# Kernel tuning notes

Measured on AMD Instinct MI355X. Metric: run time of the kernel, lower is better.

The kernel has to match this reference:

```python
import jax, jax.numpy as jnp
import numpy as np

B, S, D_IN, D_OUT = 4, 2048, 4096, 4096
ACT_CLIP = 6.0

def setup_inputs() -> dict:
    key = jax.random.key(0)
    k1, k2, k3, k4 = jax.random.split(key, 4)
    x = jax.random.normal(k1, (B, S, D_IN), dtype=jnp.float32)
    # symmetric int8 weights in [-127, 127] (stored as int8)
    weight_i8 = jax.random.randint(k2, (D_OUT, D_IN), -127, 128, dtype=jnp.int32).astype(jnp.int8)
    # per-output-channel positive scales, ~ max|w|/127 magnitude
    weight_scale = (jax.random.uniform(k3, (D_OUT,), dtype=jnp.float32) * 0.02 + 1e-4)
    bias = jax.random.normal(k4, (D_OUT,), dtype=jnp.float32)
    return {"x": x, "weight_i8": weight_i8, "weight_scale": weight_scale, "bias": bias}

def reference(x, weight_i8, weight_scale, bias):
    # activation clip
    x = jnp.clip(x, -ACT_CLIP, ACT_CLIP)
    # per-channel dequant: weight[o, i] = i8[o, i] * scale[o]
    weight = weight_i8.astype(jnp.float32) * weight_scale[:, None]
    weight = weight.astype(x.dtype)
    # F.linear: x @ weight.T + bias
    out = jnp.einsum('bsi,oi->bso', x, weight) + bias.astype(x.dtype)
    return out
```

## Files before the change

### kernel.cpp

```cpp
#include <hip/hip_runtime.h>
#include <stdint.h>
#include <stddef.h>


#define M_DIM 8192
#define N_DIM 4096
#define K_DIM 4096
#define ACT_CLIP 6.0f

#define BM 256
#define BN 128
#define BKI 64
#define NKT (K_DIM / BKI)
#define A_BYTES (BM * BKI)
#define B_BYTES (BN * BKI)
#define TILE_LDS (A_BYTES + B_BYTES)
#define RING 3

typedef __attribute__((ext_vector_type(4))) int i32x4;
typedef __attribute__((ext_vector_type(16))) int i32x16;

__device__ __forceinline__ void async_load16(const void* g, void* l) {
    __builtin_amdgcn_global_load_lds(
        (const __attribute__((address_space(1))) void*)g,
        (__attribute__((address_space(3))) void*)l, 16, 0, 0);
}

__global__ __launch_bounds__(256) void prep_kernel(
    const float* __restrict__ x, int8_t* __restrict__ xq,
    float* __restrict__ rowscale,
    const int* __restrict__ w, int8_t* __restrict__ wq) {
    const int tid = threadIdx.x;
    if (blockIdx.x < M_DIM) {
        const int row = blockIdx.x;
        const float4* xr = (const float4*)(x + (size_t)row * K_DIM);
        float4 v[4];
        float mx = 0.f;
#pragma unroll
        for (int c = 0; c < 4; ++c) {
            float4 a = xr[c * 256 + tid];
            a.x = fminf(ACT_CLIP, fmaxf(-ACT_CLIP, a.x));
            a.y = fminf(ACT_CLIP, fmaxf(-ACT_CLIP, a.y));
            a.z = fminf(ACT_CLIP, fmaxf(-ACT_CLIP, a.z));
            a.w = fminf(ACT_CLIP, fmaxf(-ACT_CLIP, a.w));
            v[c] = a;
            mx = fmaxf(mx, fmaxf(fmaxf(fabsf(a.x), fabsf(a.y)),
                                 fmaxf(fabsf(a.z), fabsf(a.w))));
        }
#pragma unroll
        for (int off = 32; off >= 1; off >>= 1)
            mx = fmaxf(mx, __shfl_xor(mx, off, 64));
        __shared__ float wmax[4];
        if ((tid & 63) == 0) wmax[tid >> 6] = mx;
        __syncthreads();
        mx = fmaxf(fmaxf(wmax[0], wmax[1]), fmaxf(wmax[2], wmax[3]));
        mx = fmaxf(mx, 1e-20f);
        const float inv = 127.f / mx;
        if (tid == 0) rowscale[row] = mx * (1.f / 127.f);
        int* out = (int*)(xq + (size_t)row * K_DIM);
#pragma unroll
        for (int c = 0; c < 4; ++c) {
            int b0 = (int)rintf(v[c].x * inv);
            int b1 = (int)rintf(v[c].y * inv);
            int b2 = (int)rintf(v[c].z * inv);
            int b3 = (int)rintf(v[c].w * inv);
            out[c * 256 + tid] =
                (b0 & 255) | ((b1 & 255) << 8) | ((b2 & 255) << 16) | ((b3 & 255) << 24);
        }
    } else {
        size_t idx = (size_t)(blockIdx.x - M_DIM) * 256 + tid;
        const int4* w4 = (const int4*)w;
        int r[4];
#pragma unroll
        for (int j = 0; j < 4; ++j) {
            int4 a = w4[idx * 4 + j];
            r[j] = (a.x & 255) | ((a.y & 255) << 8) | ((a.z & 255) << 16) |
                   ((a.w & 255) << 24);
        }
        ((int4*)wq)[idx] = make_int4(r[0], r[1], r[2], r[3]);
    }
}

__global__ __launch_bounds__(256, 2) void gemm_i8_kernel(
    const int8_t* __restrict__ A, const int8_t* __restrict__ Bw,
    const float* __restrict__ rowscale, const float* __restrict__ scale,
    const float* __restrict__ bias, float* __restrict__ out) {
    extern __shared__ __align__(16) int8_t smem[];

    const int tid = threadIdx.x;
    const int wave = tid >> 6;
    const int lane = tid & 63;
    const int l31 = lane & 31;
    const int hi = lane >> 5;
    const int m0 = blockIdx.y * BM;
    const int n0 = blockIdx.x * BN;
    const int wm = (wave >> 1) * 128;
    const int wn = (wave & 1) * 64;

    const int8_t* ga[4];
    const int8_t* gb[2];
    int lbA[4], lbB[2];
#pragma unroll
    for (int j = 0; j < 4; ++j) {
        const int s = tid + 256 * j;
        const int row = s >> 2;
        const int c = (s & 3) ^ ((row >> 1) & 3);
        ga[j] = A + (size_t)(m0 + row) * K_DIM + c * 16;
        lbA[j] = (wave * 64 + 256 * j) * 16;
    }
#pragma unroll
    for (int j = 0; j < 2; ++j) {
        const int s = tid + 256 * j;
        const int row = s >> 2;
        const int c = (s & 3) ^ ((row >> 1) & 3);
        gb[j] = Bw + (size_t)(n0 + row) * K_DIM + c * 16;
        lbB[j] = A_BYTES + (wave * 64 + 256 * j) * 16;
    }

    auto STAGE = [&](int b) {
        int8_t* buf = smem + b * TILE_LDS;
#pragma unroll
        for (int j = 0; j < 4; ++j) async_load16(ga[j], buf + lbA[j]);
#pragma unroll
        for (int j = 0; j < 2; ++j) async_load16(gb[j], buf + lbB[j]);
#pragma unroll
        for (int j = 0; j < 4; ++j) ga[j] += BKI;
#pragma unroll
        for (int j = 0; j < 2; ++j) gb[j] += BKI;
    };

    const int swz = (l31 >> 1) & 3;
    const int abase = (wm + l31) * 64;
    const int bbase = A_BYTES + (wn + l31) * 64;
    int koff[2];
#pragma unroll
    for (int ks = 0; ks < 2; ++ks) koff[ks] = ((ks * 2 + hi) ^ swz) * 16;

    i32x16 acc[4][2] = {};

    STAGE(0);
    STAGE(1);
    asm volatile("s_waitcnt vmcnt(6)" ::: "memory");
    asm volatile("s_barrier" ::: "memory");

    int cur = 0, stg = 2;
    for (int t = 0; t < NKT; ++t) {
        if (t + 2 < NKT) STAGE(stg);

        const int8_t* buf = smem + cur * TILE_LDS;
        i32x4 af[4][2], bf[2][2];
#pragma unroll
        for (int ks = 0; ks < 2; ++ks) {
#pragma unroll
            for (int mt = 0; mt < 4; ++mt)
                af[mt][ks] = *(const i32x4*)(buf + abase + mt * 2048 + koff[ks]);
#pragma unroll
            for (int nt = 0; nt < 2; ++nt)
                bf[nt][ks] = *(const i32x4*)(buf + bbase + nt * 2048 + koff[ks]);
        }
#pragma unroll
        for (int ks = 0; ks < 2; ++ks)
#pragma unroll
            for (int mt = 0; mt < 4; ++mt)
#pragma unroll
                for (int nt = 0; nt < 2; ++nt)
                    acc[mt][nt] = __builtin_amdgcn_mfma_i32_32x32x32_i8(
                        af[mt][ks], bf[nt][ks], acc[mt][nt], 0, 0, 0);

        if (t < NKT - 2) {
            asm volatile("s_waitcnt vmcnt(6)" ::: "memory");
            asm volatile("s_barrier" ::: "memory");
        } else if (t == NKT - 2) {
            asm volatile("s_waitcnt vmcnt(0)" ::: "memory");
            asm volatile("s_barrier" ::: "memory");
        }
        cur = (cur == 2) ? 0 : cur + 1;
        stg = (stg == 2) ? 0 : stg + 1;
    }

    const int ccol = l31;
#pragma unroll
    for (int mt = 0; mt < 4; ++mt) {
        const int gmb = m0 + wm + mt * 32;
        float rs[16];
#pragma unroll
        for (int r = 0; r < 16; ++r)
            rs[r] = rowscale[gmb + (r & 3) + 4 * hi + 8 * (r >> 2)];
#pragma unroll
        for (int nt = 0; nt < 2; ++nt) {
            const int gn = n0 + wn + nt * 32 + ccol;
            const float sc = scale[gn];
            const float bi = bias[gn];
            float* op = out + (size_t)gmb * N_DIM + gn;
#pragma unroll
            for (int r = 0; r < 16; ++r) {
                const int grow = (r & 3) + 4 * hi + 8 * (r >> 2);
                op[(size_t)grow * N_DIM] =
                    fmaf((float)acc[mt][nt][r], rs[r] * sc, bi);
            }
        }
    }
}

extern "C" void kernel_launch(void* const* d_in, const int* in_sizes, int n_in,
                              void* d_out, int out_size, void* d_ws, size_t ws_size,
                              hipStream_t stream) {
    const float* x = (const float*)d_in[0];
    const int* w_i8 = (const int*)d_in[1];
    const float* w_scale = (const float*)d_in[2];
    const float* bias = (const float*)d_in[3];
    float* out = (float*)d_out;

    int8_t* xq = (int8_t*)d_ws;
    int8_t* wq = (int8_t*)d_ws + (size_t)M_DIM * K_DIM;
    float* rowscale = (float*)((int8_t*)d_ws + (size_t)M_DIM * K_DIM
                               + (size_t)N_DIM * K_DIM);

    static bool attr_done = false;
    if (!attr_done) {
        hipFuncSetAttribute((const void*)gemm_i8_kernel,
                            hipFuncAttributeMaxDynamicSharedMemorySize,
                            RING * TILE_LDS);
        attr_done = true;
    }

    const int pack_blocks = (int)((size_t)N_DIM * K_DIM / (16 * 256));
    prep_kernel<<<M_DIM + pack_blocks, 256, 0, stream>>>(x, xq, rowscale, w_i8, wq);

    dim3 grid(N_DIM / BN, M_DIM / BM);
    gemm_i8_kernel<<<grid, 256, RING * TILE_LDS, stream>>>(
        xq, wq, rowscale, w_scale, bias, out);
}
```

Before: 413.1 us.

## Pre-tile int8 operands into MFMA fragment layout and load directly to registers

The prep kernel now writes quantized activations and packed weights in a blocked layout: 32-row blocks where each 16-byte lane chunk matches the MFMA operand fragment. The GEMM kernel drops the LDS ring buffer, the async global-to-LDS copies and the barriers. It loads fragments straight from global memory into registers with software double buffering. This removes LDS traffic and synchronisation, but each wave refetches its A/B tiles with no sharing between waves, so L2 and global bandwidth pressure rises.

```diff
diff --git a/kernel.cpp b/kernel.cpp
--- a/kernel.cpp
+++ b/kernel.cpp
@@ -12,19 +12,10 @@
 #define BN 128
 #define BKI 64
 #define NKT (K_DIM / BKI)
-#define A_BYTES (BM * BKI)
-#define B_BYTES (BN * BKI)
-#define TILE_LDS (A_BYTES + B_BYTES)
-#define RING 3
+#define BLK_STRIDE (128 * 1024)
 
 typedef __attribute__((ext_vector_type(4))) int i32x4;
 typedef __attribute__((ext_vector_type(16))) int i32x16;
-
-__device__ __forceinline__ void async_load16(const void* g, void* l) {
-    __builtin_amdgcn_global_load_lds(
-        (const __attribute__((address_space(1))) void*)g,
-        (__attribute__((address_space(3))) void*)l, 16, 0, 0);
-}
 
 __global__ __launch_bounds__(256) void prep_kernel(
     const float* __restrict__ x, int8_t* __restrict__ xq,
@@ -32,13 +23,14 @@
     const int* __restrict__ w, int8_t* __restrict__ wq) {
     const int tid = threadIdx.x;
     if (blockIdx.x < M_DIM) {
-        const int row = blockIdx.x;
+        const int g = blockIdx.x >> 8, i = blockIdx.x & 255;
+        const int row = g * 256 + (i & 7) * 32 + (i >> 3);
         const float4* xr = (const float4*)(x + (size_t)row * K_DIM);
         float4 v[4];
         float mx = 0.f;
 #pragma unroll
         for (int c = 0; c < 4; ++c) {
-            float4 a = xr[c * 256 + tid];
+            float4 a = xr[tid * 4 + c];
             a.x = fminf(ACT_CLIP, fmaxf(-ACT_CLIP, a.x));
             a.y = fminf(ACT_CLIP, fmaxf(-ACT_CLIP, a.y));
             a.z = fminf(ACT_CLIP, fmaxf(-ACT_CLIP, a.z));
@@ -57,36 +49,41 @@
         mx = fmaxf(mx, 1e-20f);
         const float inv = 127.f / mx;
         if (tid == 0) rowscale[row] = mx * (1.f / 127.f);
-        int* out = (int*)(xq + (size_t)row * K_DIM);
+        int bo[4];
 #pragma unroll
         for (int c = 0; c < 4; ++c) {
             int b0 = (int)rintf(v[c].x * inv);
             int b1 = (int)rintf(v[c].y * inv);
             int b2 = (int)rintf(v[c].z * inv);
             int b3 = (int)rintf(v[c].w * inv);
-            out[c * 256 + tid] =
-                (b0 & 255) | ((b1 & 255) << 8) | ((b2 & 255) << 16) | ((b3 & 255) << 24);
+            bo[c] = (b0 & 255) | ((b1 & 255) << 8) | ((b2 & 255) << 16) |
+                    ((b3 & 255) << 24);
         }
+        int8_t* dst = xq + ((size_t)(row >> 5) * 128 + (tid >> 1)) * 1024 +
+                      (row & 31) * 16 + (tid & 1) * 512;
+        *(int4*)dst = make_int4(bo[0], bo[1], bo[2], bo[3]);
     } else {
-        size_t idx = (size_t)(blockIdx.x - M_DIM) * 256 + tid;
-        const int4* w4 = (const int4*)w;
-        int r[4];
+        const int pb = blockIdx.x - M_DIM;
+        const int g = pb >> 8, i = pb & 255;
+        const int n = g * 256 + (i & 7) * 32 + (i >> 3);
+        const int4* w4 = (const int4*)(w + (size_t)n * K_DIM);
+        int bo[4];
 #pragma unroll
         for (int j = 0; j < 4; ++j) {
-            int4 a = w4[idx * 4 + j];
-            r[j] = (a.x & 255) | ((a.y & 255) << 8) | ((a.z & 255) << 16) |
-                   ((a.w & 255) << 24);
+            int4 a = w4[tid * 4 + j];
+            bo[j] = (a.x & 255) | ((a.y & 255) << 8) | ((a.z & 255) << 16) |
+                    ((a.w & 255) << 24);
         }
-        ((int4*)wq)[idx] = make_int4(r[0], r[1], r[2], r[3]);
+        int8_t* dst = wq + ((size_t)(n >> 5) * 128 + (tid >> 1)) * 1024 +
+                      (n & 31) * 16 + (tid & 1) * 512;
+        *(int4*)dst = make_int4(bo[0], bo[1], bo[2], bo[3]);
     }
 }
 
 __global__ __launch_bounds__(256, 2) void gemm_i8_kernel(
-    const int8_t* __restrict__ A, const int8_t* __restrict__ Bw,
+    const int8_t* __restrict__ At, const int8_t* __restrict__ Bt,
     const float* __restrict__ rowscale, const float* __restrict__ scale,
     const float* __restrict__ bias, float* __restrict__ out) {
-    extern __shared__ __align__(16) int8_t smem[];
-
     const int tid = threadIdx.x;
     const int wave = tid >> 6;
     const int lane = tid & 63;
@@ -97,86 +94,55 @@
     const int wm = (wave >> 1) * 128;
     const int wn = (wave & 1) * 64;
 
-    const int8_t* ga[4];
-    const int8_t* gb[2];
-    int lbA[4], lbB[2];
+    const int8_t* pa[4];
+    const int8_t* pb[2];
 #pragma unroll
-    for (int j = 0; j < 4; ++j) {
-        const int s = tid + 256 * j;
-        const int row = s >> 2;
-        const int c = (s & 3) ^ ((row >> 1) & 3);
-        ga[j] = A + (size_t)(m0 + row) * K_DIM + c * 16;
-        lbA[j] = (wave * 64 + 256 * j) * 16;
-    }
+    for (int mt = 0; mt < 4; ++mt)
+        pa[mt] = At + (size_t)(((m0 + wm) >> 5) + mt) * BLK_STRIDE + lane * 16;
 #pragma unroll
-    for (int j = 0; j < 2; ++j) {
-        const int s = tid + 256 * j;
-        const int row = s >> 2;
-        const int c = (s & 3) ^ ((row >> 1) & 3);
-        gb[j] = Bw + (size_t)(n0 + row) * K_DIM + c * 16;
-        lbB[j] = A_BYTES + (wave * 64 + 256 * j) * 16;
-    }
+    for (int nt = 0; nt < 2; ++nt)
+        pb[nt] = Bt + (size_t)(((n0 + wn) >> 5) + nt) * BLK_STRIDE + lane * 16;
 
-    auto STAGE = [&](int b) {
-        int8_t* buf = smem + b * TILE_LDS;
-#pragma unroll
-        for (int j = 0; j < 4; ++j) async_load16(ga[j], buf + lbA[j]);
-#pragma unroll
-        for (int j = 0; j < 2; ++j) async_load16(gb[j], buf + lbB[j]);
-#pragma unroll
-        for (int j = 0; j < 4; ++j) ga[j] += BKI;
-#pragma unroll
-        for (int j = 0; j < 2; ++j) gb[j] += BKI;
-    };
-
-    const int swz = (l31 >> 1) & 3;
-    const int abase = (wm + l31) * 64;
-    const int bbase = A_BYTES + (wn + l31) * 64;
-    int koff[2];
-#pragma unroll
-    for (int ks = 0; ks < 2; ++ks) koff[ks] = ((ks * 2 + hi) ^ swz) * 16;
-
+    i32x4 aX[8], bX[4], aY[8], bY[4];
     i32x16 acc[4][2] = {};
 
-    STAGE(0);
-    STAGE(1);
-    asm volatile("s_waitcnt vmcnt(6)" ::: "memory");
-    asm volatile("s_barrier" ::: "memory");
+#define LOADT(af, bf)                                                  \
+    do {                                                               \
+        _Pragma("unroll") for (int mt = 0; mt < 4; ++mt) {             \
+            af[mt * 2 + 0] = *(const i32x4*)(pa[mt]);                  \
+            af[mt * 2 + 1] = *(const i32x4*)(pa[mt] + 1024);           \
+        }                                                              \
+        _Pragma("unroll") for (int nt = 0; nt < 2; ++nt) {             \
+            bf[nt * 2 + 0] = *(const i32x4*)(pb[nt]);                  \
+            bf[nt * 2 + 1] = *(const i32x4*)(pb[nt] + 1024);           \
+        }                                                              \
+        _Pragma("unroll") for (int mt = 0; mt < 4; ++mt) pa[mt] += 2048; \
+        _Pragma("unroll") for (int nt = 0; nt < 2; ++nt) pb[nt] += 2048; \
+    } while (0)
 
-    int cur = 0, stg = 2;
-    for (int t = 0; t < NKT; ++t) {
-        if (t + 2 < NKT) STAGE(stg);
+#define MFMAT(af, bf)                                                  \
+    do {                                                               \
+        _Pragma("unroll") for (int ks = 0; ks < 2; ++ks)               \
+            _Pragma("unroll") for (int mt = 0; mt < 4; ++mt)           \
+                _Pragma("unroll") for (int nt = 0; nt < 2; ++nt)       \
+                    acc[mt][nt] = __builtin_amdgcn_mfma_i32_32x32x32_i8( \
+                        af[mt * 2 + ks], bf[nt * 2 + ks], acc[mt][nt], \
+                        0, 0, 0);                                      \
+    } while (0)
 
-        const int8_t* buf = smem + cur * TILE_LDS;
-        i32x4 af[4][2], bf[2][2];
-#pragma unroll
-        for (int ks = 0; ks < 2; ++ks) {
-#pragma unroll
-            for (int mt = 0; mt < 4; ++mt)
-                af[mt][ks] = *(const i32x4*)(buf + abase + mt * 2048 + koff[ks]);
-#pragma unroll
-            for (int nt = 0; nt < 2; ++nt)
-                bf[nt][ks] = *(const i32x4*)(buf + bbase + nt * 2048 + koff[ks]);
-        }
-#pragma unroll
-        for (int ks = 0; ks < 2; ++ks)
-#pragma unroll
-            for (int mt = 0; mt < 4; ++mt)
-#pragma unroll
-                for (int nt = 0; nt < 2; ++nt)
-                    acc[mt][nt] = __builtin_amdgcn_mfma_i32_32x32x32_i8(
-                        af[mt][ks], bf[nt][ks], acc[mt][nt], 0, 0, 0);
+    LOADT(aX, bX);
+    for (int t = 0; t < NKT - 2; t += 2) {
+        LOADT(aY, bY);
+        MFMAT(aX, bX);
+        LOADT(aX, bX);
+        MFMAT(aY, bY);
+    }
+    LOADT(aY, bY);
+    MFMAT(aX, bX);
+    MFMAT(aY, bY);
 
-        if (t < NKT - 2) {
-            asm volatile("s_waitcnt vmcnt(6)" ::: "memory");
-            asm volatile("s_barrier" ::: "memory");
-        } else if (t == NKT - 2) {
-            asm volatile("s_waitcnt vmcnt(0)" ::: "memory");
-            asm volatile("s_barrier" ::: "memory");
-        }
-        cur = (cur == 2) ? 0 : cur + 1;
-        stg = (stg == 2) ? 0 : stg + 1;
-    }
+#undef LOADT
+#undef MFMAT
 
     const int ccol = l31;
 #pragma unroll
@@ -216,18 +182,9 @@
     float* rowscale = (float*)((int8_t*)d_ws + (size_t)M_DIM * K_DIM
                                + (size_t)N_DIM * K_DIM);
 
-    static bool attr_done = false;
-    if (!attr_done) {
-        hipFuncSetAttribute((const void*)gemm_i8_kernel,
-                            hipFuncAttributeMaxDynamicSharedMemorySize,
-                            RING * TILE_LDS);
-        attr_done = true;
-    }
-
-    const int pack_blocks = (int)((size_t)N_DIM * K_DIM / (16 * 256));
-    prep_kernel<<<M_DIM + pack_blocks, 256, 0, stream>>>(x, xq, rowscale, w_i8, wq);
+    prep_kernel<<<M_DIM + N_DIM, 256, 0, stream>>>(x, xq, rowscale, w_i8, wq);
 
     dim3 grid(N_DIM / BN, M_DIM / BM);
-    gemm_i8_kernel<<<grid, 256, RING * TILE_LDS, stream>>>(
+    gemm_i8_kernel<<<grid, 256, 0, stream>>>(
         xq, wq, rowscale, w_scale, bias, out);
 }
```

Result: no change. 411.1 us (-0.5%).
